# Performance work log

Measured on AMD Instinct MI355X. Metric: run time of the kernel, lower is better.

## Reference

```python
import jax, jax.numpy as jnp
from jax import lax
import numpy as np

B, C_IN, HW = 4096, 3, 32
D = 256          # feature/output dim
E = 16           # num experts
H = 1024         # expert hidden dim
K = 2            # top-k
NC = 1000        # num classes


def _conv(x, w, b):
    # x: NCHW, w: OIHW, stride 1, SAME padding
    y = lax.conv_general_dilated(x, w, (1, 1), 'SAME',
                                 dimension_numbers=('NCHW', 'OIHW', 'NCHW'))
    return y + b[None, :, None, None]


def _maxpool2(x):
    return lax.reduce_window(x, -jnp.inf, lax.max, (1, 1, 2, 2), (1, 1, 2, 2), 'VALID')


def setup_inputs() -> dict:
    key = jax.random.key(0)
    ks = jax.random.split(key, 16)
    s = lambda *sh: 1.0 / np.sqrt(sh[-2] if len(sh) > 1 else sh[0])
    inp = {
        'x':       jax.random.normal(ks[0], (B, C_IN, HW, HW), jnp.float32),
        'conv1_w': jax.random.normal(ks[1], (32, 3, 3, 3), jnp.float32) * 0.1,
        'conv1_b': jnp.zeros((32,), jnp.float32),
        'conv2_w': jax.random.normal(ks[2], (64, 32, 3, 3), jnp.float32) * 0.05,
        'conv2_b': jnp.zeros((64,), jnp.float32),
        'conv3_w': jax.random.normal(ks[3], (128, 64, 3, 3), jnp.float32) * 0.04,
        'conv3_b': jnp.zeros((128,), jnp.float32),
        'fc_w':    jax.random.normal(ks[4], (128 * 4 * 4, D), jnp.float32) * (1.0 / np.sqrt(2048)),
        'fc_b':    jnp.zeros((D,), jnp.float32),
        'gate_w':  jax.random.normal(ks[5], (D, E), jnp.float32) * (1.0 / np.sqrt(D)),
        'gate_b':  jnp.zeros((E,), jnp.float32),
        'e_w1':    jax.random.normal(ks[6], (E, D, H), jnp.float32) * (1.0 / np.sqrt(D)),
        'e_b1':    jnp.zeros((E, H), jnp.float32),
        'e_w2':    jax.random.normal(ks[7], (E, H, D), jnp.float32) * (1.0 / np.sqrt(H)),
        'e_b2':    jnp.zeros((E, D), jnp.float32),
        'ln_g':    jnp.ones((D,), jnp.float32),
        'ln_b':    jnp.zeros((D,), jnp.float32),
        'out_w':   jax.random.normal(ks[8], (D, NC), jnp.float32) * (1.0 / np.sqrt(D)),
        'out_b':   jnp.zeros((NC,), jnp.float32),
    }
    return inp


def reference(x, conv1_w, conv1_b, conv2_w, conv2_b, conv3_w, conv3_b,
              fc_w, fc_b, gate_w, gate_b, e_w1, e_b1, e_w2, e_b2,
              ln_g, ln_b, out_w, out_b):
    # --- CNN feature extractor: conv -> maxpool -> relu, x3 ---
    h = jax.nn.relu(_maxpool2(_conv(x, conv1_w, conv1_b)))   # [B,32,16,16]
    h = jax.nn.relu(_maxpool2(_conv(h, conv2_w, conv2_b)))   # [B,64,8,8]
    h = jax.nn.relu(_maxpool2(_conv(h, conv3_w, conv3_b)))   # [B,128,4,4]
    feat = h.reshape(h.shape[0], -1) @ fc_w + fc_b           # [B,D]

    # --- Gating: top-k softmax scattered into sparse [B,E] ---
    logits = feat @ gate_w + gate_b                          # [B,E]
    topk_vals, topk_idx = lax.top_k(logits, K)               # [B,K]
    gate_w_k = jax.nn.softmax(topk_vals, axis=-1)            # [B,K]
    gates = jnp.zeros_like(logits).at[jnp.arange(feat.shape[0])[:, None], topk_idx].set(gate_w_k)

    # --- Dense all-expert compute, masked combine (faithful to source) ---
    h1 = jax.nn.relu(jnp.einsum('bd,edh->beh', feat, e_w1) + e_b1[None])   # [B,E,H]
    eo = jnp.einsum('beh,ehd->bed', h1, e_w2) + e_b2[None]                 # [B,E,D]
    moe = jnp.einsum('be,bed->bd', gates, eo)                              # [B,D]

    D_i = gates.mean(axis=0)
    lb_loss = jnp.sum(D_i * jnp.log(D_i + 1e-8))

    # --- LayerNorm(residual) ---
    y = moe + feat
    mu = y.mean(-1, keepdims=True)
    var = y.var(-1, keepdims=True)
    y = (y - mu) / jnp.sqrt(var + 1e-5) * ln_g + ln_b

    out = y @ out_w + out_b                                   # [B,NC]
    return out, lb_loss
```

## Files before the change

kernel.cpp:

```cpp
#include <hip/hip_runtime.h>
#include <hip/hip_bf16.h>

typedef short bf16x8 __attribute__((ext_vector_type(8)));
typedef float f32x4 __attribute__((ext_vector_type(4)));

#define NB   4096
#define NEXP 16
#define DDIM 256
#define HDIM 1024
#define NCLS 1000

#define OFF_B    ((size_t)0)
#define OFF_P0   ((size_t)0)
#define OFF_P1   ((size_t)4194304)
#define OFF_W1TH ((size_t)8388608)
#define OFF_W1TL ((size_t)16777216)
#define OFF_W2TH ((size_t)25165824)
#define OFF_W2TL ((size_t)33554432)
#define OFF_WFCH ((size_t)41943040)
#define OFF_WFCL ((size_t)42991616)
#define OFF_P2   ((size_t)44040192)
#define OFF_P3   ((size_t)48234496)
#define OFF_OWH  ((size_t)52428800)
#define OFF_OWL  ((size_t)53477376)
#define OFF_CHH  ((size_t)67108864)
#define OFF_CHL  ((size_t)83886080)
#define OFF_WBL  ((size_t)67145728)
#define OFF_WA1H ((size_t)67182592)
#define OFF_WA1L ((size_t)67184640)
#define OFF_FEAT ((size_t)100663296)
#define OFF_WAL  ((size_t)100810752)
#define OFF_MOE  ((size_t)104857600)
#define OFF_CNT  ((size_t)109051904)
#define OFF_GSUM ((size_t)109051968)
#define OFF_LROW ((size_t)109052032)
#define OFF_LG   ((size_t)109314176)
#define OFF2_W1TH ((size_t)109600768)
#define OFF2_W1TL ((size_t)117989376)
#define OFF2_W2TH ((size_t)126377984)
#define OFF2_W2TL ((size_t)134766592)
#define OFF2_WFCH ((size_t)143155200)
#define OFF2_WFCL ((size_t)144203776)
#define OFF2_OWH  ((size_t)145252352)
#define OFF2_OWL  ((size_t)146300928)
#define WS_BIG    ((size_t)147349504)

__device__ inline unsigned short f2bf(float v) {
  __hip_bfloat16 h = __float2bfloat16(v);
  return *(unsigned short*)&h;
}
__device__ inline float bf2f(unsigned short u) {
  union { unsigned int i; float f; } c; c.i = ((unsigned int)u) << 16; return c.f;
}

__global__ __launch_bounds__(256) void k_wprep(
    const float* __restrict__ c1w, unsigned short* __restrict__ a1h, unsigned short* __restrict__ a1l,
    const float* __restrict__ c2w, unsigned short* __restrict__ b2h, unsigned short* __restrict__ b2l,
    const float* __restrict__ c3w, unsigned short* __restrict__ a3h, unsigned short* __restrict__ a3l) {
  int i = blockIdx.x*256 + threadIdx.x;
  if (i < 1024) {
    int k = i & 31, oc = i >> 5;
    float v = (k < 27) ? c1w[oc*27 + k] : 0.f;
    unsigned short h = f2bf(v);
    a1h[i] = h; a1l[i] = f2bf(v - bf2f(h));
  } else if (i < 19456) {
    int j = i - 1024;
    int ic = j & 31, rem = j >> 5;
    int oc = rem & 63, tap = rem >> 6;
    float v = c2w[(oc*32 + ic)*9 + tap];
    unsigned short h = f2bf(v);
    b2h[j] = h; b2l[j] = f2bf(v - bf2f(h));
  } else if (i < 93184) {
    int j = i - 19456;
    int ic = j & 63, rem = j >> 6;
    int oc = rem & 127, tap = rem >> 7;
    float v = c3w[(oc*64 + ic)*9 + tap];
    unsigned short h = f2bf(v);
    a3h[j] = h; a3l[j] = f2bf(v - bf2f(h));
  }
}

__device__ inline void pack_body(const float* __restrict__ in,
    unsigned short* __restrict__ oh, unsigned short* __restrict__ ol,
    int R, int C, int bx, int by, int e, int t, float (*tile)[65]) {
  const size_t eb = (size_t)e * R * C;
  const int c0 = bx*64, r0 = by*64;
  const int cc = t & 63, r4 = t >> 6;
  #pragma unroll
  for (int j = 0; j < 16; ++j) {
    int rr = r4 + j*4;
    tile[rr][cc] = in[eb + (size_t)(r0+rr)*C + c0 + cc];
  }
  __syncthreads();
  const int K32 = R >> 5;
  #pragma unroll
  for (int j = 0; j < 16; ++j) {
    int idx = t + j*256;
    int jin = idx & 7, lane = (idx >> 3) & 63, ksl = (idx >> 9) & 1, ntl = idx >> 10;
    int kl = ksl*32 + ((lane >> 4) << 3) + jin;
    int nl = ntl*16 + (lane & 15);
    float v = tile[kl][nl];
    unsigned short h = f2bf(v);
    size_t o = eb + ((size_t)(((c0 >> 4) + ntl)*K32 + (r0 >> 5) + ksl)*64 + lane)*8 + jin;
    oh[o] = h;
    ol[o] = f2bf(v - bf2f(h));
  }
}

__device__ inline void pack_dispatch(int b, int t, float (*tile)[65],
    const float* __restrict__ ew1, unsigned short* __restrict__ w1th, unsigned short* __restrict__ w1tl,
    const float* __restrict__ ew2, unsigned short* __restrict__ w2th, unsigned short* __restrict__ w2tl,
    const float* __restrict__ fcw, unsigned short* __restrict__ wfh,  unsigned short* __restrict__ wfl,
    const float* __restrict__ ow,  unsigned short* __restrict__ owh,  unsigned short* __restrict__ owl) {
  if (b < 1024) {
    int bx = b & 15, by = (b >> 4) & 3, e = b >> 6;
    pack_body(ew1, w1th, w1tl, 256, 1024, bx, by, e, t, tile);
  } else if (b < 2048) {
    int lb = b - 1024;
    int bx = lb & 3, by = (lb >> 2) & 15, e = lb >> 6;
    pack_body(ew2, w2th, w2tl, 1024, 256, bx, by, e, t, tile);
  } else if (b < 2176) {
    int lb = b - 2048;
    int bx = lb & 3, by = lb >> 2;
    pack_body(fcw, wfh, wfl, 2048, 256, bx, by, 0, t, tile);
  } else {
    int lb = b - 2176;
    int i = lb*256 + t;
    int j = i & 7, lane = (i >> 3) & 63, ks = (i >> 9) & 7, nt = i >> 12;
    int k = ks*32 + ((lane >> 4) << 3) + j;
    int n = nt*16 + (lane & 15);
    float v = (n < NCLS) ? ow[(size_t)k*NCLS + n] : 0.f;
    unsigned short h = f2bf(v);
    owh[i] = h;
    owl[i] = f2bf(v - bf2f(h));
  }
}

__global__ __launch_bounds__(256) void k_packall(
    const float* __restrict__ ew1, unsigned short* __restrict__ w1th, unsigned short* __restrict__ w1tl,
    const float* __restrict__ ew2, unsigned short* __restrict__ w2th, unsigned short* __restrict__ w2tl,
    const float* __restrict__ fcw, unsigned short* __restrict__ wfh,  unsigned short* __restrict__ wfl,
    const float* __restrict__ ow,  unsigned short* __restrict__ owh,  unsigned short* __restrict__ owl) {
  __shared__ float tile[64][65];
  pack_dispatch(blockIdx.x, threadIdx.x, tile,
                ew1, w1th, w1tl, ew2, w2th, w2tl, fcw, wfh, wfl, ow, owh, owl);
}

__global__ __launch_bounds__(512, 4) void k_conv12(const float* __restrict__ x,
    const unsigned short* __restrict__ wA1h, const unsigned short* __restrict__ wA1l,
    const float* __restrict__ b1,
    const unsigned short* __restrict__ wBh, const unsigned short* __restrict__ wBl,
    const float* __restrict__ b2, float* __restrict__ outB) {
  __shared__ unsigned int xsu[3*34*36 + 1152];
  __shared__ __align__(16) unsigned short ishB[2][12960];
  __shared__ float bs1[32];
  __shared__ float bs2[64];
  const int t = threadIdx.x;
  const int img = blockIdx.x;
  for (int i = t; i < 3*34*36 + 1152; i += 512) xsu[i] = 0u;
  {
    unsigned int* z = (unsigned int*)&ishB[0][0];
    for (int i = t; i < 2720; i += 512) {
      int plane = i / 1360, rem = i - plane*1360;
      int b = rem / 20, o = rem - b*20;
      int pl;
      if (b < 18)      pl = b;
      else if (b < 36) pl = 306 + (b - 18);
      else if (b < 52) pl = (b - 35) * 18;
      else             pl = (b - 51) * 18 + 17;
      z[plane*6480 + pl*20 + o] = 0u;
    }
  }
  __syncthreads();
  for (int i = t; i < 3072; i += 512) {
    int ic = i >> 10, rem = i & 1023, y = rem >> 5, xx = rem & 31;
    float v = x[(size_t)img*3072 + i];
    unsigned short h = f2bf(v);
    unsigned short l = f2bf(v - bf2f(h));
    xsu[ic*34*36 + (y+1)*36 + (xx+1)] = ((unsigned int)l << 16) | (unsigned int)h;
  }
  if (t < 32) bs1[t] = b1[t];
  else if (t >= 64 && t < 128) bs2[t-64] = b2[t-64];

  const int lane = t & 63, wvv = t >> 6;
  const int lr = lane & 15, lq = lane >> 4;

  const int oct1 = wvv & 1;
  const bf16x8 a1h = *(const bf16x8*)&wA1h[((oct1*16 + lr) << 5) + lq*8];
  const bf16x8 a1l = *(const bf16x8*)&wA1l[((oct1*16 + lr) << 5) + lq*8];

  int koff[8];
  #pragma unroll
  for (int j = 0; j < 8; ++j) {
    int k = lq*8 + j;
    if (k < 27) {
      int ic = k/9, tap = k - ic*9, dy = tap/3, dx = tap - dy*3;
      koff[j] = ic*34*36 + dy*36 + dx;
    } else koff[j] = 3*34*36;
  }
  __syncthreads();

  {
    const int rp  = wvv >> 1;
    const int ly0 = (rp >> 1) << 1;
    const int xh  = rp & 1;
    const int X   = xh*16 + lr;
    for (int ps = 0; ps < 8; ++ps) {
      const int baseA = (ps*4 + ly0)*36 + X;
      f32x4 aA = (f32x4){0.f,0.f,0.f,0.f}, aB = (f32x4){0.f,0.f,0.f,0.f};
      {
        union { unsigned int u[4]; bf16x8 v; } bh_, bl_;
        #pragma unroll
        for (int jj = 0; jj < 4; ++jj) {
          unsigned int e0 = xsu[koff[2*jj]   + baseA];
          unsigned int e1 = xsu[koff[2*jj+1] + baseA];
          bh_.u[jj] = __builtin_amdgcn_perm(e1, e0, 0x05040100u);
          bl_.u[jj] = __builtin_amdgcn_perm(e1, e0, 0x07060302u);
        }
        aA = __builtin_amdgcn_mfma_f32_16x16x32_bf16(a1h, bh_.v, aA, 0, 0, 0);
        aA = __builtin_amdgcn_mfma_f32_16x16x32_bf16(a1h, bl_.v, aA, 0, 0, 0);
        aA = __builtin_amdgcn_mfma_f32_16x16x32_bf16(a1l, bh_.v, aA, 0, 0, 0);
      }
      {
        union { unsigned int u[4]; bf16x8 v; } bh_, bl_;
        #pragma unroll
        for (int jj = 0; jj < 4; ++jj) {
          unsigned int e0 = xsu[koff[2*jj]   + baseA + 36];
          unsigned int e1 = xsu[koff[2*jj+1] + baseA + 36];
          bh_.u[jj] = __builtin_amdgcn_perm(e1, e0, 0x05040100u);
          bl_.u[jj] = __builtin_amdgcn_perm(e1, e0, 0x07060302u);
        }
        aB = __builtin_amdgcn_mfma_f32_16x16x32_bf16(a1h, bh_.v, aB, 0, 0, 0);
        aB = __builtin_amdgcn_mfma_f32_16x16x32_bf16(a1h, bl_.v, aB, 0, 0, 0);
        aB = __builtin_amdgcn_mfma_f32_16x16x32_bf16(a1l, bh_.v, aB, 0, 0, 0);
      }
      #pragma unroll
      for (int r = 0; r < 4; ++r) {
        float v = fmaxf(aA[r], aB[r]);
        v = fmaxf(v, __shfl_xor(v, 1, 64));
        if ((lr & 1) == 0) {
          int oc = oct1*16 + lq*4 + r;
          int Xp = xh*8 + (lr >> 1);
          int Yp = ps*2 + (ly0 >> 1);
          float m = fmaxf(v + bs1[oc], 0.f);
          unsigned short h = f2bf(m);
          unsigned short l = f2bf(m - bf2f(h));
          int pl = (Yp+1)*18 + (Xp+1);
          int us = (pl*5 + (oc >> 3))*8 + (oc & 7);
          ishB[0][us] = h; ishB[1][us] = l;
        }
      }
    }
  }
  __syncthreads();
  {
    const int mtp = (wvv & 1)*2;
    const int rq = wvv >> 1;
    f32x4 acc[2][4];
    #pragma unroll
    for (int i = 0; i < 2; ++i)
      #pragma unroll
      for (int j = 0; j < 4; ++j) acc[i][j] = (f32x4){0.f,0.f,0.f,0.f};
    #pragma unroll
    for (int tap = 0; tap < 9; ++tap) {
      const int off0 = ((tap*64 + mtp*16     + lr) << 5) + lq*8;
      const int off1 = ((tap*64 + (mtp+1)*16 + lr) << 5) + lq*8;
      bf16x8 ah0 = *(const bf16x8*)&wBh[off0];
      bf16x8 al0 = *(const bf16x8*)&wBl[off0];
      bf16x8 ah1 = *(const bf16x8*)&wBh[off1];
      bf16x8 al1 = *(const bf16x8*)&wBl[off1];
      const int dy = tap/3, dx = tap - dy*3;
      #pragma unroll
      for (int j = 0; j < 4; ++j) {
        int pl = (rq*4 + j + dy)*18 + lr + dx;
        int slot = pl*5 + lq;
        bf16x8 bh = *(const bf16x8*)&ishB[0][slot << 3];
        bf16x8 bl = *(const bf16x8*)&ishB[1][slot << 3];
        acc[0][j] = __builtin_amdgcn_mfma_f32_16x16x32_bf16(ah0, bh, acc[0][j], 0, 0, 0);
        acc[1][j] = __builtin_amdgcn_mfma_f32_16x16x32_bf16(ah1, bh, acc[1][j], 0, 0, 0);
        acc[0][j] = __builtin_amdgcn_mfma_f32_16x16x32_bf16(ah0, bl, acc[0][j], 0, 0, 0);
        acc[1][j] = __builtin_amdgcn_mfma_f32_16x16x32_bf16(ah1, bl, acc[1][j], 0, 0, 0);
        acc[0][j] = __builtin_amdgcn_mfma_f32_16x16x32_bf16(al0, bh, acc[0][j], 0, 0, 0);
        acc[1][j] = __builtin_amdgcn_mfma_f32_16x16x32_bf16(al1, bh, acc[1][j], 0, 0, 0);
      }
    }
    __syncthreads();
    float* ps2 = (float*)&ishB[0][0];
    #pragma unroll
    for (int m = 0; m < 2; ++m)
      #pragma unroll
      for (int k = 0; k < 2; ++k)
        #pragma unroll
        for (int r = 0; r < 4; ++r) {
          float v = fmaxf(acc[m][2*k][r], acc[m][2*k+1][r]);
          v = fmaxf(v, __shfl_xor(v, 1, 64));
          if ((lr & 1) == 0) {
            int oc = (mtp + m)*16 + lq*4 + r;
            int Y = rq*2 + k, X = lr >> 1;
            ps2[oc*65 + Y*8 + X] = fmaxf(v + bs2[oc], 0.f);
          }
        }
    __syncthreads();
    float* op = outB + (size_t)img*4096;
    #pragma unroll
    for (int jj = 0; jj < 8; ++jj) {
      int i = jj*512 + t;
      op[i] = ps2[(i >> 6)*65 + (i & 63)];
    }
  }
}

__global__ __launch_bounds__(256) void k_conv3(const float* __restrict__ inB,
    const unsigned short* __restrict__ wAh, const unsigned short* __restrict__ wAl,
    const float* __restrict__ bias,
    unsigned short* __restrict__ Chh, unsigned short* __restrict__ Chl,
    const float* __restrict__ ew1, unsigned short* __restrict__ w1th, unsigned short* __restrict__ w1tl,
    const float* __restrict__ ew2, unsigned short* __restrict__ w2th, unsigned short* __restrict__ w2tl,
    const float* __restrict__ fcw, unsigned short* __restrict__ wfh,  unsigned short* __restrict__ wfl,
    const float* __restrict__ ow,  unsigned short* __restrict__ owh,  unsigned short* __restrict__ owl) {
  __shared__ unsigned short ish[2][6400];
  const int t = threadIdx.x;
  if (blockIdx.x >= 4096) {
    float (*tile)[65] = (float(*)[65])&ish[0][0];
    pack_dispatch(blockIdx.x - 4096, t, tile,
                  ew1, w1th, w1tl, ew2, w2th, w2tl, fcw, wfh, wfl, ow, owh, owl);
    return;
  }
  const int img = blockIdx.x;
  {
    unsigned int* z = (unsigned int*)&ish[0][0];
    #pragma unroll
    for (int j = 0; j < 25; ++j) z[t + 256*j] = 0u;
  }
  __syncthreads();
  {
    const float* src = inB + (size_t)img*4096;
    #pragma unroll
    for (int j = 0; j < 16; ++j) {
      int f = t + 256*j;
      int ic = f >> 6, p = f & 63;
      int pl = ((p >> 3) + 1)*10 + (p & 7) + 1;
      float v = src[f];
      unsigned short h = f2bf(v);
      unsigned short l = f2bf(v - bf2f(h));
      int u = pl*64 + ic;
      int us = (((u >> 3) ^ (pl & 7)) << 3) | (u & 7);
      ish[0][us] = h; ish[1][us] = l;
    }
  }
  __syncthreads();

  const int lane = t & 63, wid = t >> 6;
  const int lr = lane & 15, lq = lane >> 4;
  const int mt0 = wid*2;
  const int yb = lr >> 3, xb = lr & 7;
  const int wrow0 = (mt0*16 + lr) << 6;
  const int wrow1 = ((mt0+1)*16 + lr) << 6;

  f32x4 acc[2][4];
  #pragma unroll
  for (int i = 0; i < 2; ++i)
    #pragma unroll
    for (int j = 0; j < 4; ++j) acc[i][j] = (f32x4){0.f,0.f,0.f,0.f};

  bf16x8 a0h, a0l, a1h, a1l;
  {
    const int wb = lq*8;
    a0h = *(const bf16x8*)&wAh[wb + wrow0];
    a0l = *(const bf16x8*)&wAl[wb + wrow0];
    a1h = *(const bf16x8*)&wAh[wb + wrow1];
    a1l = *(const bf16x8*)&wAl[wb + wrow1];
  }
  for (int it = 0; it < 18; ++it) {
    const int tap = it >> 1, kc = it & 1;
    bf16x8 n0h, n0l, n1h, n1l;
    if (it < 17) {
      const int tap2 = (it+1) >> 1, kc2 = (it+1) & 1;
      const int wb2 = ((tap2 << 7) << 6) + kc2*32 + lq*8;
      n0h = *(const bf16x8*)&wAh[wb2 + wrow0];
      n0l = *(const bf16x8*)&wAl[wb2 + wrow0];
      n1h = *(const bf16x8*)&wAh[wb2 + wrow1];
      n1l = *(const bf16x8*)&wAl[wb2 + wrow1];
    }
    const int dy = tap/3, dx = tap - dy*3;
    const int kb = kc*32 + lq*8;
    #pragma unroll
    for (int nt = 0; nt < 4; ++nt) {
      const int pl = (2*nt + yb + dy)*10 + xb + dx;
      const int u = pl*64 + kb;
      const int us = (((u >> 3) ^ (pl & 7)) << 3);
      bf16x8 bh = *(const bf16x8*)&ish[0][us];
      bf16x8 bl = *(const bf16x8*)&ish[1][us];
      acc[0][nt] = __builtin_amdgcn_mfma_f32_16x16x32_bf16(a0h, bh, acc[0][nt], 0, 0, 0);
      acc[0][nt] = __builtin_amdgcn_mfma_f32_16x16x32_bf16(a0h, bl, acc[0][nt], 0, 0, 0);
      acc[0][nt] = __builtin_amdgcn_mfma_f32_16x16x32_bf16(a0l, bh, acc[0][nt], 0, 0, 0);
      acc[1][nt] = __builtin_amdgcn_mfma_f32_16x16x32_bf16(a1h, bh, acc[1][nt], 0, 0, 0);
      acc[1][nt] = __builtin_amdgcn_mfma_f32_16x16x32_bf16(a1h, bl, acc[1][nt], 0, 0, 0);
      acc[1][nt] = __builtin_amdgcn_mfma_f32_16x16x32_bf16(a1l, bh, acc[1][nt], 0, 0, 0);
    }
    if (it < 17) { a0h = n0h; a0l = n0l; a1h = n1h; a1l = n1l; }
  }
  __syncthreads();
  float* stg = (float*)&ish[0][0];
  #pragma unroll
  for (int mtl = 0; mtl < 2; ++mtl)
    #pragma unroll
    for (int nt = 0; nt < 4; ++nt)
      #pragma unroll
      for (int r = 0; r < 4; ++r) {
        float v = acc[mtl][nt][r];
        v = fmaxf(v, __shfl_xor(v, 1, 64));
        v = fmaxf(v, __shfl_xor(v, 8, 64));
        if ((lane & 9) == 0) {
          int oc = (mt0 + mtl)*16 + lq*4 + r;
          int pix = nt*4 + (xb >> 1);
          stg[oc*17 + pix] = fmaxf(v + bias[oc], 0.f);
        }
      }
  __syncthreads();
  #pragma unroll
  for (int j = 0; j < 8; ++j) {
    int i = t + 256*j;
    float v = stg[(i >> 4)*17 + (i & 15)];
    unsigned short h = f2bf(v);
    Chh[(size_t)img*2048 + i] = h;
    Chl[(size_t)img*2048 + i] = f2bf(v - bf2f(h));
  }
}

__global__ __launch_bounds__(256) void k_fc(const unsigned short* __restrict__ Chh,
    const unsigned short* __restrict__ Chl,
    const unsigned short* __restrict__ wfh, const unsigned short* __restrict__ wfl,
    float* __restrict__ P0, float* __restrict__ P1,
    float* __restrict__ P2, float* __restrict__ P3) {
  const int t = threadIdx.x;
  const int r0 = blockIdx.x * 32;
  const int kq = blockIdx.z;
  float* __restrict__ P = (kq == 0) ? P0 : (kq == 1) ? P1 : (kq == 2) ? P2 : P3;
  const int lane = t & 63, wv = t >> 6;
  const int lr = lane & 15, lq = lane >> 4;
  f32x4 acc[2][4];
  #pragma unroll
  for (int i = 0; i < 2; ++i)
    #pragma unroll
    for (int j = 0; j < 4; ++j) acc[i][j] = (f32x4){0.f,0.f,0.f,0.f};
  bf16x8 ah[2], al[2], bh[4], bl[4];
  #pragma unroll
  for (int rt = 0; rt < 2; ++rt) {
    size_t ao = (size_t)(r0 + rt*16 + lr)*2048 + kq*512 + lq*8;
    ah[rt] = *(const bf16x8*)&Chh[ao];
    al[rt] = *(const bf16x8*)&Chl[ao];
  }
  #pragma unroll
  for (int nt = 0; nt < 4; ++nt) {
    size_t bo = ((size_t)((wv*4 + nt)*64 + kq*16)*64 + lane)*8;
    bh[nt] = *(const bf16x8*)&wfh[bo];
    bl[nt] = *(const bf16x8*)&wfl[bo];
  }
  #pragma unroll 4
  for (int ks = 0; ks < 16; ++ks) {
    bf16x8 nah[2], nal[2], nbh[4], nbl[4];
    if (ks < 15) {
      #pragma unroll
      for (int rt = 0; rt < 2; ++rt) {
        size_t ao = (size_t)(r0 + rt*16 + lr)*2048 + kq*512 + (ks+1)*32 + lq*8;
        nah[rt] = *(const bf16x8*)&Chh[ao];
        nal[rt] = *(const bf16x8*)&Chl[ao];
      }
      #pragma unroll
      for (int nt = 0; nt < 4; ++nt) {
        size_t bo = ((size_t)((wv*4 + nt)*64 + kq*16 + ks + 1)*64 + lane)*8;
        nbh[nt] = *(const bf16x8*)&wfh[bo];
        nbl[nt] = *(const bf16x8*)&wfl[bo];
      }
    }
    #pragma unroll
    for (int nt = 0; nt < 4; ++nt) {
      acc[0][nt] = __builtin_amdgcn_mfma_f32_16x16x32_bf16(ah[0], bh[nt], acc[0][nt], 0, 0, 0);
      acc[1][nt] = __builtin_amdgcn_mfma_f32_16x16x32_bf16(ah[1], bh[nt], acc[1][nt], 0, 0, 0);
      acc[0][nt] = __builtin_amdgcn_mfma_f32_16x16x32_bf16(ah[0], bl[nt], acc[0][nt], 0, 0, 0);
      acc[1][nt] = __builtin_amdgcn_mfma_f32_16x16x32_bf16(ah[1], bl[nt], acc[1][nt], 0, 0, 0);
      acc[0][nt] = __builtin_amdgcn_mfma_f32_16x16x32_bf16(al[0], bh[nt], acc[0][nt], 0, 0, 0);
      acc[1][nt] = __builtin_amdgcn_mfma_f32_16x16x32_bf16(al[1], bh[nt], acc[1][nt], 0, 0, 0);
    }
    if (ks < 15) {
      #pragma unroll
      for (int rt = 0; rt < 2; ++rt) { ah[rt] = nah[rt]; al[rt] = nal[rt]; }
      #pragma unroll
      for (int nt = 0; nt < 4; ++nt) { bh[nt] = nbh[nt]; bl[nt] = nbl[nt]; }
    }
  }
  #pragma unroll
  for (int rt = 0; rt < 2; ++rt)
    #pragma unroll
    for (int nt = 0; nt < 4; ++nt)
      #pragma unroll
      for (int r = 0; r < 4; ++r)
        P[(size_t)(r0 + rt*16 + lq*4 + r)*256 + (wv*4 + nt)*16 + lr] = acc[rt][nt][r];
}

__global__ __launch_bounds__(256) void k_gate(const float* __restrict__ P0,
    const float* __restrict__ P1, const float* __restrict__ P2, const float* __restrict__ P3,
    const float* __restrict__ fcb,
    const float* __restrict__ gw, const float* __restrict__ gb,
    float* __restrict__ feat, int* __restrict__ cnt, float* __restrict__ gsum,
    int* __restrict__ lrow, float* __restrict__ lg) {
  __shared__ float ft[16][256];
  __shared__ float lgs[16][16];
  __shared__ float gwl[4096];
  const int t = threadIdx.x;
  const int r0 = blockIdx.x * 16;
  for (int i = t; i < 4096; i += 256) gwl[i] = gw[i];
  float bb = fcb[t];
  #pragma unroll
  for (int r = 0; r < 16; ++r) {
    size_t off = (size_t)(r0+r)*256 + t;
    float v = P0[off] + P1[off] + P2[off] + P3[off] + bb;
    ft[r][t] = v;
    feat[off] = v;
  }
  __syncthreads();
  {
    int r = t >> 4, e = t & 15;
    float s = gb[e];
    for (int k = 0; k < 256; ++k) s = fmaf(ft[r][k], gwl[k*16 + e], s);
    lgs[r][e] = s;
  }
  __syncthreads();
  if (t < 16) {
    int r = t;
    float v1 = -3.402823e38f, v2 = -3.402823e38f;
    int i1 = 0, i2 = 0;
    for (int e = 0; e < 16; ++e) {
      float v = lgs[r][e];
      if (v > v1)      { v2 = v1; i2 = i1; v1 = v; i1 = e; }
      else if (v > v2) { v2 = v;  i2 = e; }
    }
    float ex = __expf(v2 - v1);
    float g1 = 1.f / (1.f + ex);
    float g2 = ex  / (1.f + ex);
    int row = r0 + r;
    int p1 = atomicAdd(&cnt[i1], 1); lrow[i1*4096 + p1] = row; lg[i1*4096 + p1] = g1;
    int p2 = atomicAdd(&cnt[i2], 1); lrow[i2*4096 + p2] = row; lg[i2*4096 + p2] = g2;
    atomicAdd(&gsum[i1], g1);
    atomicAdd(&gsum[i2], g2);
  }
}

__global__ __launch_bounds__(256) void k_moe(const float* __restrict__ feat,
    const unsigned short* __restrict__ w1th, const unsigned short* __restrict__ w1tl,
    const unsigned short* __restrict__ w2th, const unsigned short* __restrict__ w2tl,
    const float* __restrict__ eb1, const float* __restrict__ eb2,
    const int* __restrict__ cnt, const int* __restrict__ lrow, const float* __restrict__ lgw,
    float* __restrict__ moe) {
  const int e = blockIdx.y;
  const int n_e = cnt[e];
  const int start = blockIdx.x * 32;
  if (start >= n_e) return;
  const int c = blockIdx.z;
  const int n = min(32, n_e - start);
  __shared__ unsigned short fh[8192], fl[8192];
  __shared__ unsigned short h1h[4096], h1l[4096];
  __shared__ int   rws[32];
  __shared__ float gws[32];
  const int t = threadIdx.x;
  if (t < 32) {
    rws[t] = (t < n) ? lrow[e*4096 + start + t] : 0;
    gws[t] = (t < n) ? lgw[e*4096 + start + t] : 0.f;
  }
  __syncthreads();
  for (int j = 0; j < 32; ++j) {
    float v = (j < n) ? feat[(size_t)rws[j]*256 + t] : 0.f;
    unsigned short h = f2bf(v);
    int us = (j*32 + ((t >> 3) ^ (j & 7)))*8 + (t & 7);
    fh[us] = h; fl[us] = f2bf(v - bf2f(h));
  }
  const int lane = t & 63, wv = t >> 6;
  const int lr = lane & 15, lq = lane >> 4;
  const int rh = wv & 1, qh = wv >> 1;
  const int arow = rh*16 + lr;
  const int rsw = arow & 7;
  const size_t ewb = (size_t)e << 18;

  f32x4 acc2[8];
  #pragma unroll
  for (int i = 0; i < 8; ++i) acc2[i] = (f32x4){0.f,0.f,0.f,0.f};

  __syncthreads();

  {
    f32x4 acc1[4];
    #pragma unroll
    for (int i = 0; i < 4; ++i) acc1[i] = (f32x4){0.f,0.f,0.f,0.f};
    bf16x8 wbh[4], wbl[4];
    #pragma unroll
    for (int ht = 0; ht < 4; ++ht) {
      size_t bo = ewb + ((size_t)((c*8 + qh*4 + ht)*8 + 0)*64 + lane)*8;
      wbh[ht] = *(const bf16x8*)&w1th[bo];
      wbl[ht] = *(const bf16x8*)&w1tl[bo];
    }
    #pragma unroll
    for (int ks = 0; ks < 8; ++ks) {
      bf16x8 nbh[4], nbl[4];
      if (ks < 7) {
        #pragma unroll
        for (int ht = 0; ht < 4; ++ht) {
          size_t bo = ewb + ((size_t)((c*8 + qh*4 + ht)*8 + ks + 1)*64 + lane)*8;
          nbh[ht] = *(const bf16x8*)&w1th[bo];
          nbl[ht] = *(const bf16x8*)&w1tl[bo];
        }
      }
      int aoff = (arow*32 + ((ks*4 + lq) ^ rsw))*8;
      bf16x8 ah = *(const bf16x8*)&fh[aoff];
      bf16x8 al = *(const bf16x8*)&fl[aoff];
      #pragma unroll
      for (int ht = 0; ht < 4; ++ht) {
        acc1[ht] = __builtin_amdgcn_mfma_f32_16x16x32_bf16(ah, wbh[ht], acc1[ht], 0, 0, 0);
        acc1[ht] = __builtin_amdgcn_mfma_f32_16x16x32_bf16(ah, wbl[ht], acc1[ht], 0, 0, 0);
        acc1[ht] = __builtin_amdgcn_mfma_f32_16x16x32_bf16(al, wbh[ht], acc1[ht], 0, 0, 0);
      }
      if (ks < 7) {
        #pragma unroll
        for (int ht = 0; ht < 4; ++ht) { wbh[ht] = nbh[ht]; wbl[ht] = nbl[ht]; }
      }
    }
    __syncthreads();
    #pragma unroll
    for (int ht = 0; ht < 4; ++ht) {
      int hloc = qh*64 + ht*16 + lr;
      float bb = eb1[e*1024 + c*128 + hloc];
      #pragma unroll
      for (int r = 0; r < 4; ++r) {
        int orow = rh*16 + lq*4 + r;
        float v = fmaxf(acc1[ht][r] + bb, 0.f);
        unsigned short hh = f2bf(v);
        int us = (orow*16 + ((hloc >> 3) ^ (orow & 7)))*8 + (hloc & 7);
        h1h[us] = hh; h1l[us] = f2bf(v - bf2f(hh));
      }
    }
    __syncthreads();
    bf16x8 w2h[4], w2l[4];
    #pragma unroll
    for (int dt = 0; dt < 4; ++dt) {
      size_t bo = ewb + ((size_t)((qh*8 + dt)*32 + c*4 + 0)*64 + lane)*8;
      w2h[dt] = *(const bf16x8*)&w2th[bo];
      w2l[dt] = *(const bf16x8*)&w2tl[bo];
    }
    #pragma unroll
    for (int g = 0; g < 8; ++g) {
      const int ks = g >> 1, dth = (g & 1)*4;
      bf16x8 nh[4], nl[4];
      if (g < 7) {
        const int ks2 = (g+1) >> 1, dth2 = ((g+1) & 1)*4;
        #pragma unroll
        for (int dt = 0; dt < 4; ++dt) {
          size_t bo = ewb + ((size_t)((qh*8 + dth2 + dt)*32 + c*4 + ks2)*64 + lane)*8;
          nh[dt] = *(const bf16x8*)&w2th[bo];
          nl[dt] = *(const bf16x8*)&w2tl[bo];
        }
      }
      int aoff = (arow*16 + ((ks*4 + lq) ^ rsw))*8;
      bf16x8 ah = *(const bf16x8*)&h1h[aoff];
      bf16x8 al = *(const bf16x8*)&h1l[aoff];
      #pragma unroll
      for (int dt = 0; dt < 4; ++dt) {
        acc2[dth+dt] = __builtin_amdgcn_mfma_f32_16x16x32_bf16(ah, w2h[dt], acc2[dth+dt], 0, 0, 0);
        acc2[dth+dt] = __builtin_amdgcn_mfma_f32_16x16x32_bf16(ah, w2l[dt], acc2[dth+dt], 0, 0, 0);
        acc2[dth+dt] = __builtin_amdgcn_mfma_f32_16x16x32_bf16(al, w2h[dt], acc2[dth+dt], 0, 0, 0);
      }
      if (g < 7) {
        #pragma unroll
        for (int dt = 0; dt < 4; ++dt) { w2h[dt] = nh[dt]; w2l[dt] = nl[dt]; }
      }
    }
  }
  #pragma unroll
  for (int dt = 0; dt < 8; ++dt) {
    int d = qh*128 + dt*16 + lr;
    float b2 = (c == 0) ? eb2[e*256 + d] : 0.f;
    #pragma unroll
    for (int r = 0; r < 4; ++r) {
      int orow = rh*16 + lq*4 + r;
      if (orow < n)
        atomicAdd(&moe[(size_t)rws[orow]*256 + d], gws[orow]*(acc2[dt][r] + b2));
    }
  }
}

__global__ __launch_bounds__(256) void k_ln(const float* __restrict__ feat,
    const float* __restrict__ moe, const float* __restrict__ g, const float* __restrict__ bp,
    unsigned short* __restrict__ yh, unsigned short* __restrict__ yl,
    const float* __restrict__ gsum, float* __restrict__ out_lb) {
  const int r = blockIdx.x, t = threadIdx.x;
  if (r == NB) {
    if (t < 64) {
      float term = 0.f;
      if (t < 16) {
        float D = gsum[t] * (1.f/4096.f);
        term = D * logf(D + 1e-8f);
      }
      #pragma unroll
      for (int o = 8; o > 0; o >>= 1) term += __shfl_down(term, o, 64);
      if (t == 0) *out_lb = term;
    }
    return;
  }
  float v = moe[(size_t)r*256 + t] + feat[(size_t)r*256 + t];
  float s = v, q = v * v;
  #pragma unroll
  for (int o = 32; o > 0; o >>= 1) {
    s += __shfl_down(s, o, 64);
    q += __shfl_down(q, o, 64);
  }
  __shared__ float ss[4], qq[4];
  int wv = t >> 6;
  if ((t & 63) == 0) { ss[wv] = s; qq[wv] = q; }
  __syncthreads();
  float S = ss[0]+ss[1]+ss[2]+ss[3];
  float Q = qq[0]+qq[1]+qq[2]+qq[3];
  float mu  = S * (1.f/256.f);
  float var = Q * (1.f/256.f) - mu*mu;
  float inv = rsqrtf(var + 1e-5f);
  float y = (v - mu) * inv * g[t] + bp[t];
  unsigned short h = f2bf(y);
  yh[(size_t)r*256 + t] = h;
  yl[(size_t)r*256 + t] = f2bf(y - bf2f(h));
}

__global__ __launch_bounds__(256) void k_out(const unsigned short* __restrict__ yh,
    const unsigned short* __restrict__ yl,
    const unsigned short* __restrict__ owh, const unsigned short* __restrict__ owl,
    const float* __restrict__ ob, float* __restrict__ out) {
  const int t = threadIdx.x;
  const int r0 = blockIdx.x * 32;
  const int lane = t & 63, wv = t >> 6;
  const int lr = lane & 15, lq = lane >> 4;
  const int ntile = blockIdx.y*4 + wv;
  f32x4 acc[2];
  acc[0] = (f32x4){0.f,0.f,0.f,0.f};
  acc[1] = (f32x4){0.f,0.f,0.f,0.f};
  bf16x8 bh, bl, ah[2], al[2];
  {
    size_t bo = ((size_t)(ntile*8)*64 + lane)*8;
    bh = *(const bf16x8*)&owh[bo];
    bl = *(const bf16x8*)&owl[bo];
  }
  #pragma unroll
  for (int rt = 0; rt < 2; ++rt) {
    size_t ao = (size_t)(r0 + rt*16 + lr)*256 + lq*8;
    ah[rt] = *(const bf16x8*)&yh[ao];
    al[rt] = *(const bf16x8*)&yl[ao];
  }
  #pragma unroll
  for (int ks = 0; ks < 8; ++ks) {
    bf16x8 nbh, nbl, nah[2], nal[2];
    if (ks < 7) {
      size_t bo = ((size_t)(ntile*8 + ks + 1)*64 + lane)*8;
      nbh = *(const bf16x8*)&owh[bo];
      nbl = *(const bf16x8*)&owl[bo];
      #pragma unroll
      for (int rt = 0; rt < 2; ++rt) {
        size_t ao = (size_t)(r0 + rt*16 + lr)*256 + (ks+1)*32 + lq*8;
        nah[rt] = *(const bf16x8*)&yh[ao];
        nal[rt] = *(const bf16x8*)&yl[ao];
      }
    }
    #pragma unroll
    for (int rt = 0; rt < 2; ++rt) {
      acc[rt] = __builtin_amdgcn_mfma_f32_16x16x32_bf16(ah[rt], bh, acc[rt], 0, 0, 0);
      acc[rt] = __builtin_amdgcn_mfma_f32_16x16x32_bf16(ah[rt], bl, acc[rt], 0, 0, 0);
      acc[rt] = __builtin_amdgcn_mfma_f32_16x16x32_bf16(al[rt], bh, acc[rt], 0, 0, 0);
    }
    if (ks < 7) {
      bh = nbh; bl = nbl;
      #pragma unroll
      for (int rt = 0; rt < 2; ++rt) { ah[rt] = nah[rt]; al[rt] = nal[rt]; }
    }
  }
  const int col = ntile*16 + lr;
  if (col < NCLS) {
    float bb = ob[col];
    #pragma unroll
    for (int rt = 0; rt < 2; ++rt)
      #pragma unroll
      for (int r = 0; r < 4; ++r)
        out[(size_t)(r0 + rt*16 + lq*4 + r)*NCLS + col] = acc[rt][r] + bb;
  }
}

extern "C" void kernel_launch(void* const* d_in, const int* in_sizes, int n_in,
                              void* d_out, int out_size, void* d_ws, size_t ws_size,
                              hipStream_t stream) {
  const float* x   = (const float*)d_in[0];
  const float* c1w = (const float*)d_in[1];
  const float* c1b = (const float*)d_in[2];
  const float* c2w = (const float*)d_in[3];
  const float* c2b = (const float*)d_in[4];
  const float* c3w = (const float*)d_in[5];
  const float* c3b = (const float*)d_in[6];
  const float* fcw = (const float*)d_in[7];
  const float* fcb = (const float*)d_in[8];
  const float* gw  = (const float*)d_in[9];
  const float* gb  = (const float*)d_in[10];
  const float* ew1 = (const float*)d_in[11];
  const float* eb1 = (const float*)d_in[12];
  const float* ew2 = (const float*)d_in[13];
  const float* eb2 = (const float*)d_in[14];
  const float* lng = (const float*)d_in[15];
  const float* lnb = (const float*)d_in[16];
  const float* ow  = (const float*)d_in[17];
  const float* ob  = (const float*)d_in[18];
  char* ws = (char*)d_ws;
  const bool bigws = ws_size >= WS_BIG;
  const size_t oW1TH = bigws ? OFF2_W1TH : OFF_W1TH;
  const size_t oW1TL = bigws ? OFF2_W1TL : OFF_W1TL;
  const size_t oW2TH = bigws ? OFF2_W2TH : OFF_W2TH;
  const size_t oW2TL = bigws ? OFF2_W2TL : OFF_W2TL;
  const size_t oWFCH = bigws ? OFF2_WFCH : OFF_WFCH;
  const size_t oWFCL = bigws ? OFF2_WFCL : OFF_WFCL;
  const size_t oOWH  = bigws ? OFF2_OWH  : OFF_OWH;
  const size_t oOWL  = bigws ? OFF2_OWL  : OFF_OWL;

  float* Bb   = (float*)(ws + OFF_B);
  float* P0   = (float*)(ws + OFF_P0);
  float* P1   = (float*)(ws + OFF_P1);
  float* P2   = (float*)(ws + OFF_P2);
  float* P3   = (float*)(ws + OFF_P3);
  unsigned short* Chh = (unsigned short*)(ws + OFF_CHH);
  unsigned short* Chl = (unsigned short*)(ws + OFF_CHL);
  unsigned short* wBh = (unsigned short*)(ws + OFF_CHH);
  unsigned short* wBl = (unsigned short*)(ws + OFF_WBL);
  unsigned short* wA1h = (unsigned short*)(ws + OFF_WA1H);
  unsigned short* wA1l = (unsigned short*)(ws + OFF_WA1L);
  unsigned short* wAh = (unsigned short*)(ws + OFF_FEAT);
  unsigned short* wAl = (unsigned short*)(ws + OFF_WAL);
  unsigned short* w1th = (unsigned short*)(ws + oW1TH);
  unsigned short* w1tl = (unsigned short*)(ws + oW1TL);
  unsigned short* w2th = (unsigned short*)(ws + oW2TH);
  unsigned short* w2tl = (unsigned short*)(ws + oW2TL);
  unsigned short* wfh = (unsigned short*)(ws + oWFCH);
  unsigned short* wfl = (unsigned short*)(ws + oWFCL);
  unsigned short* owph = (unsigned short*)(ws + oOWH);
  unsigned short* owpl = (unsigned short*)(ws + oOWL);
  unsigned short* yh = (unsigned short*)(ws + OFF_P0);
  unsigned short* yl = (unsigned short*)(ws + OFF_P1);
  float* feat = (float*)(ws + OFF_FEAT);
  float* moe  = (float*)(ws + OFF_MOE);
  int*   cnt  = (int*)(ws + OFF_CNT);
  float* gsum = (float*)(ws + OFF_GSUM);
  int*   lrow = (int*)(ws + OFF_LROW);
  float* lgv  = (float*)(ws + OFF_LG);
  float* outp = (float*)d_out;

  hipMemsetAsync(ws + OFF_MOE, 0, 4194304 + 128, stream);

  hipLaunchKernelGGL(k_wprep,  dim3(364),     dim3(256), 0, stream,
                     c1w, wA1h, wA1l, c2w, wBh, wBl, c3w, wAh, wAl);
  hipLaunchKernelGGL(k_conv12, dim3(4096),    dim3(512), 0, stream, x, wA1h, wA1l, c1b, wBh, wBl, c2b, Bb);
  hipLaunchKernelGGL(k_conv3,  dim3(bigws ? 7296 : 4096), dim3(256), 0, stream,
                     Bb, wAh, wAl, c3b, Chh, Chl,
                     ew1, w1th, w1tl, ew2, w2th, w2tl, fcw, wfh, wfl, ow, owph, owpl);
  if (!bigws)
    hipLaunchKernelGGL(k_packall, dim3(3200), dim3(256), 0, stream,
                       ew1, w1th, w1tl, ew2, w2th, w2tl, fcw, wfh, wfl, ow, owph, owpl);
  hipLaunchKernelGGL(k_fc,     dim3(128, 1, 4), dim3(256), 0, stream, Chh, Chl, wfh, wfl, P0, P1, P2, P3);
  hipLaunchKernelGGL(k_gate,   dim3(256),     dim3(256), 0, stream, P0, P1, P2, P3, fcb, gw, gb,
                     feat, cnt, gsum, lrow, lgv);
  hipLaunchKernelGGL(k_moe,    dim3(128, 16, 8), dim3(256), 0, stream, feat, w1th, w1tl, w2th, w2tl,
                     eb1, eb2, cnt, lrow, lgv, moe);
  hipLaunchKernelGGL(k_ln,     dim3(4097),    dim3(256), 0, stream, feat, moe, lng, lnb, yh, yl,
                     gsum, outp + (size_t)NB*NCLS);
  hipLaunchKernelGGL(k_out,    dim3(128, 16), dim3(256), 0, stream, yh, yl, owph, owpl, ob, outp);
}
```

Baseline: 719.2 us.

## Retile MoE expert kernel to 16-row tiles with 256-wide hidden chunks

Changes the MoE block tile from 32 token rows by 128 hidden units to 16 rows by 256 hidden units. Each wave now covers all 16 rows and a quarter of the hidden chunk, and the grid becomes 256x16x4. This cuts padding waste for experts whose token counts are not multiples of 32, halves the number of hidden-dim splits and therefore the atomic adds into the output, and lowers accumulator register use. In exchange, each block reuses every weight fragment across only 16 rows, so total weight reads from global memory double.

```diff
diff --git a/kernel.cpp b/kernel.cpp
--- a/kernel.cpp
+++ b/kernel.cpp
@@ -555,21 +555,21 @@
     float* __restrict__ moe) {
   const int e = blockIdx.y;
   const int n_e = cnt[e];
-  const int start = blockIdx.x * 32;
+  const int start = blockIdx.x * 16;
   if (start >= n_e) return;
   const int c = blockIdx.z;
-  const int n = min(32, n_e - start);
-  __shared__ unsigned short fh[8192], fl[8192];
+  const int n = min(16, n_e - start);
+  __shared__ unsigned short fh[4096], fl[4096];
   __shared__ unsigned short h1h[4096], h1l[4096];
-  __shared__ int   rws[32];
-  __shared__ float gws[32];
+  __shared__ int   rws[16];
+  __shared__ float gws[16];
   const int t = threadIdx.x;
-  if (t < 32) {
+  if (t < 16) {
     rws[t] = (t < n) ? lrow[e*4096 + start + t] : 0;
     gws[t] = (t < n) ? lgw[e*4096 + start + t] : 0.f;
   }
   __syncthreads();
-  for (int j = 0; j < 32; ++j) {
+  for (int j = 0; j < 16; ++j) {
     float v = (j < n) ? feat[(size_t)rws[j]*256 + t] : 0.f;
     unsigned short h = f2bf(v);
     int us = (j*32 + ((t >> 3) ^ (j & 7)))*8 + (t & 7);
@@ -577,25 +577,20 @@
   }
   const int lane = t & 63, wv = t >> 6;
   const int lr = lane & 15, lq = lane >> 4;
-  const int rh = wv & 1, qh = wv >> 1;
-  const int arow = rh*16 + lr;
+  const int arow = lr;
   const int rsw = arow & 7;
   const size_t ewb = (size_t)e << 18;
 
-  f32x4 acc2[8];
-  #pragma unroll
-  for (int i = 0; i < 8; ++i) acc2[i] = (f32x4){0.f,0.f,0.f,0.f};
-
-  __syncthreads();
-
-  {
-    f32x4 acc1[4];
-    #pragma unroll
-    for (int i = 0; i < 4; ++i) acc1[i] = (f32x4){0.f,0.f,0.f,0.f};
+  __syncthreads();
+
+  f32x4 acc1[4];
+  #pragma unroll
+  for (int i = 0; i < 4; ++i) acc1[i] = (f32x4){0.f,0.f,0.f,0.f};
+  {
     bf16x8 wbh[4], wbl[4];
     #pragma unroll
     for (int ht = 0; ht < 4; ++ht) {
-      size_t bo = ewb + ((size_t)((c*8 + qh*4 + ht)*8 + 0)*64 + lane)*8;
+      size_t bo = ewb + ((size_t)((c*16 + wv*4 + ht)*8 + 0)*64 + lane)*8;
       wbh[ht] = *(const bf16x8*)&w1th[bo];
       wbl[ht] = *(const bf16x8*)&w1tl[bo];
     }
@@ -605,7 +600,7 @@
       if (ks < 7) {
         #pragma unroll
         for (int ht = 0; ht < 4; ++ht) {
-          size_t bo = ewb + ((size_t)((c*8 + qh*4 + ht)*8 + ks + 1)*64 + lane)*8;
+          size_t bo = ewb + ((size_t)((c*16 + wv*4 + ht)*8 + ks + 1)*64 + lane)*8;
           nbh[ht] = *(const bf16x8*)&w1th[bo];
           nbl[ht] = *(const bf16x8*)&w1tl[bo];
         }
@@ -624,63 +619,66 @@
         for (int ht = 0; ht < 4; ++ht) { wbh[ht] = nbh[ht]; wbl[ht] = nbl[ht]; }
       }
     }
-    __syncthreads();
-    #pragma unroll
-    for (int ht = 0; ht < 4; ++ht) {
-      int hloc = qh*64 + ht*16 + lr;
-      float bb = eb1[e*1024 + c*128 + hloc];
-      #pragma unroll
-      for (int r = 0; r < 4; ++r) {
-        int orow = rh*16 + lq*4 + r;
-        float v = fmaxf(acc1[ht][r] + bb, 0.f);
-        unsigned short hh = f2bf(v);
-        int us = (orow*16 + ((hloc >> 3) ^ (orow & 7)))*8 + (hloc & 7);
-        h1h[us] = hh; h1l[us] = f2bf(v - bf2f(hh));
-      }
-    }
-    __syncthreads();
+  }
+  __syncthreads();
+  #pragma unroll
+  for (int ht = 0; ht < 4; ++ht) {
+    int hloc = wv*64 + ht*16 + lr;
+    float bb = eb1[e*1024 + c*256 + hloc];
+    #pragma unroll
+    for (int r = 0; r < 4; ++r) {
+      int orow = lq*4 + r;
+      float v = fmaxf(acc1[ht][r] + bb, 0.f);
+      unsigned short hh = f2bf(v);
+      int us = (orow*32 + ((hloc >> 3) ^ (orow & 7)))*8 + (hloc & 7);
+      h1h[us] = hh; h1l[us] = f2bf(v - bf2f(hh));
+    }
+  }
+  __syncthreads();
+  f32x4 acc2[4];
+  #pragma unroll
+  for (int i = 0; i < 4; ++i) acc2[i] = (f32x4){0.f,0.f,0.f,0.f};
+  {
     bf16x8 w2h[4], w2l[4];
     #pragma unroll
     for (int dt = 0; dt < 4; ++dt) {
-      size_t bo = ewb + ((size_t)((qh*8 + dt)*32 + c*4 + 0)*64 + lane)*8;
+      size_t bo = ewb + ((size_t)((wv*4 + dt)*32 + c*8 + 0)*64 + lane)*8;
       w2h[dt] = *(const bf16x8*)&w2th[bo];
       w2l[dt] = *(const bf16x8*)&w2tl[bo];
     }
     #pragma unroll
-    for (int g = 0; g < 8; ++g) {
-      const int ks = g >> 1, dth = (g & 1)*4;
+    for (int ks = 0; ks < 8; ++ks) {
       bf16x8 nh[4], nl[4];
-      if (g < 7) {
-        const int ks2 = (g+1) >> 1, dth2 = ((g+1) & 1)*4;
+      if (ks < 7) {
         #pragma unroll
         for (int dt = 0; dt < 4; ++dt) {
-          size_t bo = ewb + ((size_t)((qh*8 + dth2 + dt)*32 + c*4 + ks2)*64 + lane)*8;
+          size_t bo = ewb + ((size_t)((wv*4 + dt)*32 + c*8 + ks + 1)*64 + lane)*8;
           nh[dt] = *(const bf16x8*)&w2th[bo];
           nl[dt] = *(const bf16x8*)&w2tl[bo];
         }
       }
-      int aoff = (arow*16 + ((ks*4 + lq) ^ rsw))*8;
+      int aoff = (arow*32 + ((ks*4 + lq) ^ rsw))*8;
       bf16x8 ah = *(const bf16x8*)&h1h[aoff];
       bf16x8 al = *(const bf16x8*)&h1l[aoff];
       #pragma unroll
       for (int dt = 0; dt < 4; ++dt) {
-        acc2[dth+dt] = __builtin_amdgcn_mfma_f32_16x16x32_bf16(ah, w2h[dt], acc2[dth+dt], 0, 0, 0);
-        acc2[dth+dt] = __builtin_amdgcn_mfma_f32_16x16x32_bf16(ah, w2l[dt], acc2[dth+dt], 0, 0, 0);
-        acc2[dth+dt] = __builtin_amdgcn_mfma_f32_16x16x32_bf16(al, w2h[dt], acc2[dth+dt], 0, 0, 0);
-      }
-      if (g < 7) {
+        acc2[dt] = __builtin_amdgcn_mfma_f32_16x16x32_bf16(ah, w2h[dt], acc2[dt], 0, 0, 0);
+        acc2[dt] = __builtin_amdgcn_mfma_f32_16x16x32_bf16(ah, w2l[dt], acc2[dt], 0, 0, 0);
+        acc2[dt] = __builtin_amdgcn_mfma_f32_16x16x32_bf16(al, w2h[dt], acc2[dt], 0, 0, 0);
+      }
+      if (ks < 7) {
         #pragma unroll
         for (int dt = 0; dt < 4; ++dt) { w2h[dt] = nh[dt]; w2l[dt] = nl[dt]; }
       }
     }
   }
   #pragma unroll
-  for (int dt = 0; dt < 8; ++dt) {
-    int d = qh*128 + dt*16 + lr;
+  for (int dt = 0; dt < 4; ++dt) {
+    int d = wv*64 + dt*16 + lr;
     float b2 = (c == 0) ? eb2[e*256 + d] : 0.f;
     #pragma unroll
     for (int r = 0; r < 4; ++r) {
-      int orow = rh*16 + lq*4 + r;
+      int orow = lq*4 + r;
       if (orow < n)
         atomicAdd(&moe[(size_t)rws[orow]*256 + d], gws[orow]*(acc2[dt][r] + b2));
     }
@@ -866,7 +864,7 @@
   hipLaunchKernelGGL(k_fc,     dim3(128, 1, 4), dim3(256), 0, stream, Chh, Chl, wfh, wfl, P0, P1, P2, P3);
   hipLaunchKernelGGL(k_gate,   dim3(256),     dim3(256), 0, stream, P0, P1, P2, P3, fcb, gw, gb,
                      feat, cnt, gsum, lrow, lgv);
-  hipLaunchKernelGGL(k_moe,    dim3(128, 16, 8), dim3(256), 0, stream, feat, w1th, w1tl, w2th, w2tl,
+  hipLaunchKernelGGL(k_moe,    dim3(256, 16, 4), dim3(256), 0, stream, feat, w1th, w1tl, w2th, w2tl,
                      eb1, eb2, cnt, lrow, lgv, moe);
   hipLaunchKernelGGL(k_ln,     dim3(4097),    dim3(256), 0, stream, feat, moe, lng, lnb, yh, yl,
                      gsum, outp + (size_t)NB*NCLS);
```

New measurement: 647.1 us. 1.11x faster.
